# Kernel tuning notes

Hardware: AMD Instinct MI355X
Metric: run time of the kernel (lower is better)

Reference implementation:

```python
import jax, jax.numpy as jnp
import numpy as np

# NSAFlowLayer config (from init_kwargs)
W_ORTHO = 0.5      # w: blend weight of soft-polar retraction
MAX_ITER = 50      # max_iter (run fixed-length under jit; tol check omitted)
LR = 0.1           # 'default' initial learning rate for the fidelity gradient step
NS_ITERS = 8       # Newton-Schulz iterations for the (k,k) inverse matrix sqrt
EPS = 1e-8

B, P, K = 32, 16384, 64


def _invsqrt_ns(M):
    """Differentiable inverse sqrt of SPD (k,k) matrix via coupled Newton-Schulz."""
    k = M.shape[0]
    I = jnp.eye(k, dtype=M.dtype)
    nrm = jnp.trace(M) + EPS
    Y = M / nrm
    Z = I
    for _ in range(NS_ITERS):  # small fixed loop over k x k mats
        T = 0.5 * (3.0 * I - Z @ Y)
        Y = Y @ T
        Z = T @ Z
    return Z / jnp.sqrt(nrm)  # approx M^{-1/2}


def _nsa_flow_single(x0):
    """One independent NSA flow: gradient step on 0.5||Y-X0||^2, soft-polar
    retraction toward the Stiefel manifold, nonnegativity projection."""
    def step(Y, _):
        G = Y - x0                      # fidelity gradient (p,k)
        Y = Y - LR * G                  # gradient step
        S = _invsqrt_ns(Y.T @ Y)        # (k,k) inverse sqrt of Gram matrix
        Y = (1.0 - W_ORTHO) * Y + W_ORTHO * (Y @ S)  # soft polar retraction
        Y = jnp.maximum(Y, 0.0)         # nonneg projection
        return Y, None
    Yf, _ = jax.lax.scan(step, x0, None, length=MAX_ITER)  # Y0 = X0
    return Yf


def setup_inputs() -> dict:
    key = jax.random.key(0)
    X0 = jax.random.uniform(key, (B, P, K), dtype=jnp.float32)
    return {"X0": X0}


def reference(X0) -> jnp.ndarray:
    return jax.vmap(_nsa_flow_single)(X0)  # (B, p, k)
```

## Files before the change

kernel.cpp:

```cpp
#include <hip/hip_runtime.h>


#define BATCH 32
#define NP    16384
#define NK    64
#define NITER 50
#define NSIT  8
#define EPSC  1e-8f
#define CH    64
#define NT    256
#define NTNS  512
#define SP    68

#define FMA16(D, A0, A1, A2, A3, BV) do {                                  \
  D[0][0] = fmaf(A0, BV.x, D[0][0]); D[0][1] = fmaf(A0, BV.y, D[0][1]);    \
  D[0][2] = fmaf(A0, BV.z, D[0][2]); D[0][3] = fmaf(A0, BV.w, D[0][3]);    \
  D[1][0] = fmaf(A1, BV.x, D[1][0]); D[1][1] = fmaf(A1, BV.y, D[1][1]);    \
  D[1][2] = fmaf(A1, BV.z, D[1][2]); D[1][3] = fmaf(A1, BV.w, D[1][3]);    \
  D[2][0] = fmaf(A2, BV.x, D[2][0]); D[2][1] = fmaf(A2, BV.y, D[2][1]);    \
  D[2][2] = fmaf(A2, BV.z, D[2][2]); D[2][3] = fmaf(A2, BV.w, D[2][3]);    \
  D[3][0] = fmaf(A3, BV.x, D[3][0]); D[3][1] = fmaf(A3, BV.y, D[3][1]);    \
  D[3][2] = fmaf(A3, BV.z, D[3][2]); D[3][3] = fmaf(A3, BV.w, D[3][3]);    \
} while (0)

#define FMA8(D, A0, A1, BV) do {                                           \
  D[0][0] = fmaf(A0, BV.x, D[0][0]); D[0][1] = fmaf(A0, BV.y, D[0][1]);    \
  D[0][2] = fmaf(A0, BV.z, D[0][2]); D[0][3] = fmaf(A0, BV.w, D[0][3]);    \
  D[1][0] = fmaf(A1, BV.x, D[1][0]); D[1][1] = fmaf(A1, BV.y, D[1][1]);    \
  D[1][2] = fmaf(A1, BV.z, D[1][2]); D[1][3] = fmaf(A1, BV.w, D[1][3]);    \
} while (0)

__device__ __forceinline__ void gram_acc(const float (*sZ)[SP], int i0, int j0,
                                         float (&acc)[4][4]) {
#pragma unroll 4
  for (int r = 0; r < CH; ++r) {
    float4 zi = *(const float4*)&sZ[r][i0];
    float4 zj = *(const float4*)&sZ[r][j0];
    FMA16(acc, zi.x, zi.y, zi.z, zi.w, zj);
  }
}

__global__ __launch_bounds__(NT, 4) void k_init(const float* __restrict__ X0,
                                                float* __restrict__ Y,
                                                float* __restrict__ partials,
                                                int shift) {
  __shared__ float sZ[CH][SP];
  const int tid = threadIdx.x, blk = blockIdx.x;
  const int bpb = 1 << shift;
  const int b = blk >> shift, rb = blk & (bpb - 1);
  const int rpb = NP >> shift, nch = rpb / CH;
  const size_t base = ((size_t)b * NP + (size_t)rb * rpb) * NK;
  const float* __restrict__ x0 = X0 + base;
  float* __restrict__ y = Y + base;
  const int it = tid >> 4, jt = tid & 15;
  const int i0 = it * 4, j0 = jt * 4;
  float acc[4][4] = {{0.f}};

  for (int ch = 0; ch < nch; ++ch) {
    const float* xo = x0 + ch * CH * NK;
    float* yo = y + ch * CH * NK;
#pragma unroll
    for (int q = 0; q < 4; ++q) {
      int fi = (q * NT + tid) * 4;
      float4 xv = *(const float4*)(xo + fi);
      *(float4*)(yo + fi) = xv;
      int r = fi >> 6, c = fi & 63;
      *(float4*)&sZ[r][c] = xv;
    }
    __syncthreads();
    gram_acc(sZ, i0, j0, acc);
    __syncthreads();
  }
  float* p = partials + (size_t)blk * NK * NK;
#pragma unroll
  for (int a = 0; a < 4; ++a)
    *(float4*)(p + (i0 + a) * NK + j0) =
        make_float4(acc[a][0], acc[a][1], acc[a][2], acc[a][3]);
}

__global__ __launch_bounds__(NTNS, 2) void k_ns(const float* __restrict__ partials,
                                                float* __restrict__ S,
                                                int npart) {
  __shared__ float sA[NK][SP];
  __shared__ float sB[NK][SP];
  __shared__ float sT[NK][SP];
  __shared__ float sRed[8];

  const int tid = threadIdx.x, b = blockIdx.x;
  const int it = tid >> 4, jt = tid & 15;
  const int i0 = it * 2, j0 = jt * 4;

  float m[2][4] = {{0.f}};
  const float* pb = partials + (size_t)b * npart * NK * NK;
#pragma unroll 4
  for (int p = 0; p < npart; ++p) {
    const float* pp = pb + p * NK * NK;
#pragma unroll
    for (int a = 0; a < 2; ++a) {
      float4 v = *(const float4*)(pp + (i0 + a) * NK + j0);
      m[a][0] += v.x; m[a][1] += v.y; m[a][2] += v.z; m[a][3] += v.w;
    }
  }
  float local = 0.f;
#pragma unroll
  for (int a = 0; a < 2; ++a)
#pragma unroll
    for (int c = 0; c < 4; ++c)
      if ((i0 + a) == (j0 + c)) local += m[a][c];
#pragma unroll
  for (int off = 32; off; off >>= 1) local += __shfl_down(local, off);
  if ((tid & 63) == 0) sRed[tid >> 6] = local;
  __syncthreads();
  float nrm = EPSC;
#pragma unroll
  for (int w = 0; w < 8; ++w) nrm += sRed[w];
  const float inv = 1.0f / nrm;

#pragma unroll
  for (int a = 0; a < 2; ++a)
#pragma unroll
    for (int c = 0; c < 4; ++c) {
      sA[i0 + a][j0 + c] = m[a][c] * inv;
      sB[i0 + a][j0 + c] = (i0 + a) == (j0 + c) ? 1.0f : 0.0f;
    }
  __syncthreads();

  {
#pragma unroll
    for (int a = 0; a < 2; ++a)
#pragma unroll
      for (int c = 0; c < 4; ++c)
        sT[i0 + a][j0 + c] =
            (((i0 + a) == (j0 + c)) ? 1.5f : 0.0f) - 0.5f * sA[i0 + a][j0 + c];
    __syncthreads();
    float r1[2][4] = {{0.f}};
#pragma unroll 4
    for (int k = 0; k < NK; ++k) {
      float y0 = sA[i0 + 0][k], y1 = sA[i0 + 1][k];
      float4 tv = *(const float4*)&sT[k][j0];
      FMA8(r1, y0, y1, tv);
    }
    __syncthreads();
#pragma unroll
    for (int a = 0; a < 2; ++a)
#pragma unroll
      for (int c = 0; c < 4; ++c) {
        sA[i0 + a][j0 + c] = r1[a][c];
        sB[i0 + a][j0 + c] = sT[i0 + a][j0 + c];
      }
    __syncthreads();
  }

  for (int ns = 1; ns < NSIT; ++ns) {
    float d[2][4] = {{0.f}};
#pragma unroll 4
    for (int k = 0; k < NK; ++k) {
      float b0 = sB[i0 + 0][k], b1 = sB[i0 + 1][k];
      float4 av = *(const float4*)&sA[k][j0];
      FMA8(d, b0, b1, av);
    }
#pragma unroll
    for (int a = 0; a < 2; ++a)
#pragma unroll
      for (int c = 0; c < 4; ++c)
        sT[i0 + a][j0 + c] =
            (((i0 + a) == (j0 + c)) ? 1.5f : 0.0f) - 0.5f * d[a][c];
    __syncthreads();

    float r1[2][4] = {{0.f}}, r2[2][4] = {{0.f}};
#pragma unroll 4
    for (int k = 0; k < NK; ++k) {
      float y0 = sA[i0 + 0][k], y1 = sA[i0 + 1][k];
      float4 tv = *(const float4*)&sT[k][j0];
      FMA8(r1, y0, y1, tv);
      float t0 = sT[i0 + 0][k], t1 = sT[i0 + 1][k];
      float4 zv = *(const float4*)&sB[k][j0];
      FMA8(r2, t0, t1, zv);
    }
    __syncthreads();
#pragma unroll
    for (int a = 0; a < 2; ++a)
#pragma unroll
      for (int c = 0; c < 4; ++c) {
        sA[i0 + a][j0 + c] = r1[a][c];
        sB[i0 + a][j0 + c] = r2[a][c];
      }
    __syncthreads();
  }

  const float sc = 1.0f / sqrtf(nrm);
  float* Sb = S + (size_t)b * NK * NK;
#pragma unroll
  for (int a = 0; a < 2; ++a) {
    float4 v = make_float4(sB[i0 + a][j0 + 0] * sc, sB[i0 + a][j0 + 1] * sc,
                           sB[i0 + a][j0 + 2] * sc, sB[i0 + a][j0 + 3] * sc);
    *(float4*)(Sb + (i0 + a) * NK + j0) = v;
  }
}

__global__ __launch_bounds__(NT, 4) void k_fused(const float* __restrict__ X0,
                                                 float* __restrict__ Y,
                                                 const float* __restrict__ S,
                                                 float* __restrict__ partials,
                                                 int last, int shift) {
  __shared__ float sS[NK][NK];
  __shared__ float sYp[CH][SP];

  const int tid = threadIdx.x, blk = blockIdx.x;
  const int bpb = 1 << shift;
  const int b = blk >> shift, rb = blk & (bpb - 1);
  const int rpb = NP >> shift, nch = rpb / CH;
  const size_t base = ((size_t)b * NP + (size_t)rb * rpb) * NK;
  const float* __restrict__ x0 = X0 + base;
  float* __restrict__ y = Y + base;

  {
    const float4* Sb = (const float4*)(S + (size_t)b * NK * NK);
    float4* d = (float4*)sS;
    for (int i = tid; i < NK * NK / 4; i += NT) d[i] = Sb[i];
  }

  const int it = tid >> 4, jt = tid & 15;
  const int i0 = it * 4, j0 = jt * 4;
  float acc[4][4] = {{0.f}};
  __syncthreads();

  for (int ch = 0; ch < nch; ++ch) {
    const float* xo = x0 + ch * CH * NK;
    float* yo = y + ch * CH * NK;

#pragma unroll
    for (int q = 0; q < 4; ++q) {
      int fi = (q * NT + tid) * 4;
      int r = fi >> 6, c = fi & 63;
      float4 yv = *(const float4*)(yo + fi);
      float4 xv = *(const float4*)(xo + fi);
      float4 yp;
      yp.x = fmaf(0.9f, yv.x, 0.1f * xv.x);
      yp.y = fmaf(0.9f, yv.y, 0.1f * xv.y);
      yp.z = fmaf(0.9f, yv.z, 0.1f * xv.z);
      yp.w = fmaf(0.9f, yv.w, 0.1f * xv.w);
      *(float4*)&sYp[r][c] = yp;
    }
    __syncthreads();

    float dot[4][4] = {{0.f}};
#pragma unroll 4
    for (int k = 0; k < NK; ++k) {
      float a0 = sYp[i0 + 0][k], a1 = sYp[i0 + 1][k];
      float a2 = sYp[i0 + 2][k], a3 = sYp[i0 + 3][k];
      float4 bv = *(const float4*)&sS[k][j0];
      FMA16(dot, a0, a1, a2, a3, bv);
    }
    __syncthreads();

#pragma unroll
    for (int a = 0; a < 4; ++a) {
      int r = i0 + a;
      float4 ypv = *(const float4*)&sYp[r][j0];
      float4 yn;
      yn.x = fmaxf(fmaf(0.5f, ypv.x, 0.5f * dot[a][0]), 0.f);
      yn.y = fmaxf(fmaf(0.5f, ypv.y, 0.5f * dot[a][1]), 0.f);
      yn.z = fmaxf(fmaf(0.5f, ypv.z, 0.5f * dot[a][2]), 0.f);
      yn.w = fmaxf(fmaf(0.5f, ypv.w, 0.5f * dot[a][3]), 0.f);
      *(float4*)(yo + r * NK + j0) = yn;
      if (!last) {
        float4 xv = *(const float4*)(xo + r * NK + j0);
        float4 z;
        z.x = fmaf(0.9f, yn.x, 0.1f * xv.x);
        z.y = fmaf(0.9f, yn.y, 0.1f * xv.y);
        z.z = fmaf(0.9f, yn.z, 0.1f * xv.z);
        z.w = fmaf(0.9f, yn.w, 0.1f * xv.w);
        *(float4*)&sYp[r][j0] = z;
      }
    }
    __syncthreads();
    if (!last) gram_acc(sYp, i0, j0, acc);
    __syncthreads();
  }

  if (!last) {
    float* p = partials + (size_t)blk * NK * NK;
#pragma unroll
    for (int a = 0; a < 4; ++a)
      *(float4*)(p + (i0 + a) * NK + j0) =
          make_float4(acc[a][0], acc[a][1], acc[a][2], acc[a][3]);
  }
}

extern "C" void kernel_launch(void* const* d_in, const int* in_sizes, int n_in,
                              void* d_out, int out_size, void* d_ws,
                              size_t ws_size, hipStream_t stream) {
  (void)in_sizes; (void)n_in; (void)out_size;
  const float* X0 = (const float*)d_in[0];
  float* Y = (float*)d_out;

  const size_t needed5 =
      ((size_t)(BATCH << 5) + BATCH) * NK * NK * sizeof(float);
  const int shift = (ws_size >= needed5) ? 5 : 4;
  const int nblk = BATCH << shift;

  float* partials = (float*)d_ws;
  float* S = partials + (size_t)nblk * NK * NK;

  k_init<<<nblk, NT, 0, stream>>>(X0, Y, partials, shift);
  for (int t = 0; t < NITER; ++t) {
    k_ns<<<BATCH, NTNS, 0, stream>>>(partials, S, 1 << shift);
    k_fused<<<nblk, NT, 0, stream>>>(X0, Y, S, partials,
                                     t == NITER - 1 ? 1 : 0, shift);
  }
}
```

Before: 9.877 ms.

## Add parallel partial-Gram reduction kernel and exploit Gram symmetry in fused kernel

Adds a k_red kernel that pre-reduces the per-block Gram partials into four groups per batch using 128 blocks, so k_ns, which runs only 32 blocks, sums four slots instead of all of them. In k_fused, the Gram accumulation now computes only upper-triangular 4x4 tiles, splitting each off-diagonal tile across two threads, and mirrors the results when writing to halve the FMA work. Also raises unroll factors in several inner loops. Costs an extra kernel launch per iteration and uses scattered transposed stores for the partials.

```diff
diff --git a/kernel.cpp b/kernel.cpp
--- a/kernel.cpp
+++ b/kernel.cpp
@@ -11,6 +11,7 @@
 #define NT    256
 #define NTNS  512
 #define SP    68
+#define NRED  4
 
 #define FMA16(D, A0, A1, A2, A3, BV) do {                                  \
   D[0][0] = fmaf(A0, BV.x, D[0][0]); D[0][1] = fmaf(A0, BV.y, D[0][1]);    \
@@ -32,7 +33,7 @@
 
 __device__ __forceinline__ void gram_acc(const float (*sZ)[SP], int i0, int j0,
                                          float (&acc)[4][4]) {
-#pragma unroll 4
+#pragma unroll 8
   for (int r = 0; r < CH; ++r) {
     float4 zi = *(const float4*)&sZ[r][i0];
     float4 zj = *(const float4*)&sZ[r][j0];
@@ -78,9 +79,27 @@
         make_float4(acc[a][0], acc[a][1], acc[a][2], acc[a][3]);
 }
 
+__global__ __launch_bounds__(NT, 8) void k_red(float* __restrict__ partials,
+                                               int per_group, int bpb) {
+  const int blk = blockIdx.x, tid = threadIdx.x;
+  const int b = blk >> 2, g = blk & 3;
+  float4* base = (float4*)partials +
+                 ((size_t)b * bpb + (size_t)g * per_group) * (NK * NK / 4);
+#pragma unroll
+  for (int q = 0; q < 4; ++q) {
+    int e = q * NT + tid;
+    float4 s = base[e];
+    for (int p = 1; p < per_group; ++p) {
+      float4 v = base[(size_t)p * (NK * NK / 4) + e];
+      s.x += v.x; s.y += v.y; s.z += v.z; s.w += v.w;
+    }
+    base[e] = s;
+  }
+}
+
 __global__ __launch_bounds__(NTNS, 2) void k_ns(const float* __restrict__ partials,
                                                 float* __restrict__ S,
-                                                int npart) {
+                                                int per_group, int bpb) {
   __shared__ float sA[NK][SP];
   __shared__ float sB[NK][SP];
   __shared__ float sT[NK][SP];
@@ -91,10 +110,10 @@
   const int i0 = it * 2, j0 = jt * 4;
 
   float m[2][4] = {{0.f}};
-  const float* pb = partials + (size_t)b * npart * NK * NK;
-#pragma unroll 4
-  for (int p = 0; p < npart; ++p) {
-    const float* pp = pb + p * NK * NK;
+  const float* pb = partials + (size_t)b * bpb * NK * NK;
+#pragma unroll
+  for (int g = 0; g < NRED; ++g) {
+    const float* pp = pb + (size_t)g * per_group * NK * NK;
 #pragma unroll
     for (int a = 0; a < 2; ++a) {
       float4 v = *(const float4*)(pp + (i0 + a) * NK + j0);
@@ -134,7 +153,7 @@
             (((i0 + a) == (j0 + c)) ? 1.5f : 0.0f) - 0.5f * sA[i0 + a][j0 + c];
     __syncthreads();
     float r1[2][4] = {{0.f}};
-#pragma unroll 4
+#pragma unroll 8
     for (int k = 0; k < NK; ++k) {
       float y0 = sA[i0 + 0][k], y1 = sA[i0 + 1][k];
       float4 tv = *(const float4*)&sT[k][j0];
@@ -153,7 +172,7 @@
 
   for (int ns = 1; ns < NSIT; ++ns) {
     float d[2][4] = {{0.f}};
-#pragma unroll 4
+#pragma unroll 8
     for (int k = 0; k < NK; ++k) {
       float b0 = sB[i0 + 0][k], b1 = sB[i0 + 1][k];
       float4 av = *(const float4*)&sA[k][j0];
@@ -168,7 +187,7 @@
     __syncthreads();
 
     float r1[2][4] = {{0.f}}, r2[2][4] = {{0.f}};
-#pragma unroll 4
+#pragma unroll 8
     for (int k = 0; k < NK; ++k) {
       float y0 = sA[i0 + 0][k], y1 = sA[i0 + 1][k];
       float4 tv = *(const float4*)&sT[k][j0];
@@ -222,6 +241,22 @@
 
   const int it = tid >> 4, jt = tid & 15;
   const int i0 = it * 4, j0 = jt * 4;
+
+  int g_ti, g_tj;
+  bool g_diag;
+  {
+    if (tid >= 240) { g_diag = true; g_ti = g_tj = tid - 240; }
+    else {
+      g_diag = false;
+      int p = tid >> 1;
+      int t = 0, cum = 0;
+      while (cum + (15 - t) <= p) { cum += 15 - t; ++t; }
+      g_ti = t; g_tj = t + 1 + (p - cum);
+    }
+  }
+  const int gr0 = g_ti * 4 + (g_diag ? 0 : (tid & 1) * 2);
+  const int gc0 = g_tj * 4;
+
   float acc[4][4] = {{0.f}};
   __syncthreads();
 
@@ -245,7 +280,7 @@
     __syncthreads();
 
     float dot[4][4] = {{0.f}};
-#pragma unroll 4
+#pragma unroll 8
     for (int k = 0; k < NK; ++k) {
       float a0 = sYp[i0 + 0][k], a1 = sYp[i0 + 1][k];
       float a2 = sYp[i0 + 2][k], a3 = sYp[i0 + 3][k];
@@ -275,16 +310,44 @@
       }
     }
     __syncthreads();
-    if (!last) gram_acc(sYp, i0, j0, acc);
+
+    if (!last) {
+      if (g_diag) {
+#pragma unroll 8
+        for (int r = 0; r < CH; ++r) {
+          float4 z = *(const float4*)&sYp[r][gc0];
+          FMA16(acc, z.x, z.y, z.z, z.w, z);
+        }
+      } else {
+#pragma unroll 8
+        for (int r = 0; r < CH; ++r) {
+          float a0 = sYp[r][gr0], a1 = sYp[r][gr0 + 1];
+          float4 zb = *(const float4*)&sYp[r][gc0];
+          FMA8(acc, a0, a1, zb);
+        }
+      }
+    }
     __syncthreads();
   }
 
   if (!last) {
     float* p = partials + (size_t)blk * NK * NK;
-#pragma unroll
-    for (int a = 0; a < 4; ++a)
-      *(float4*)(p + (i0 + a) * NK + j0) =
-          make_float4(acc[a][0], acc[a][1], acc[a][2], acc[a][3]);
+    if (g_diag) {
+#pragma unroll
+      for (int a = 0; a < 4; ++a)
+        *(float4*)(p + (gr0 + a) * NK + gc0) =
+            make_float4(acc[a][0], acc[a][1], acc[a][2], acc[a][3]);
+    } else {
+#pragma unroll
+      for (int a = 0; a < 2; ++a)
+        *(float4*)(p + (gr0 + a) * NK + gc0) =
+            make_float4(acc[a][0], acc[a][1], acc[a][2], acc[a][3]);
+#pragma unroll
+      for (int c = 0; c < 4; ++c) {
+        p[(gc0 + c) * NK + gr0 + 0] = acc[0][c];
+        p[(gc0 + c) * NK + gr0 + 1] = acc[1][c];
+      }
+    }
   }
 }
 
@@ -295,17 +358,20 @@
   const float* X0 = (const float*)d_in[0];
   float* Y = (float*)d_out;
 
-  const size_t needed5 =
-      ((size_t)(BATCH << 5) + BATCH) * NK * NK * sizeof(float);
+  const size_t slotf = (size_t)NK * NK;
+  const size_t needed5 = (((size_t)BATCH << 5) + BATCH) * slotf * sizeof(float);
   const int shift = (ws_size >= needed5) ? 5 : 4;
   const int nblk = BATCH << shift;
+  const int bpb = 1 << shift;
+  const int per_group = bpb / NRED;
 
   float* partials = (float*)d_ws;
-  float* S = partials + (size_t)nblk * NK * NK;
+  float* S = partials + (size_t)nblk * slotf;
 
   k_init<<<nblk, NT, 0, stream>>>(X0, Y, partials, shift);
   for (int t = 0; t < NITER; ++t) {
-    k_ns<<<BATCH, NTNS, 0, stream>>>(partials, S, 1 << shift);
+    k_red<<<BATCH * NRED, NT, 0, stream>>>(partials, per_group, bpb);
+    k_ns<<<BATCH, NTNS, 0, stream>>>(partials, S, per_group, bpb);
     k_fused<<<nblk, NT, 0, stream>>>(X0, Y, S, partials,
                                      t == NITER - 1 ? 1 : 0, shift);
   }
```

Result: slower. 10.48 ms (+6.1%).

## Use split-fp16 MFMA for Y·S and Gram accumulation in fused kernel

Applied to the files above, without the earlier changes.

Replaces the scalar FP32 FMA matmuls in the fused per-iteration kernel (Y·S projection and the Y^T Y Gram partials) with MFMA 16x16x32 fp16 instructions. Each operand is split into a hi/lo fp16 pair (lo scaled by 2048) and three MFMAs emulate near-fp32 accuracy. S is emitted by the NS kernel as transposed hi/lo fp16 arrays. It also bumps a few unroll factors. The extra conversion work, the transposed LDS stores (likely bank conflicts), and the reduced precision are traded for matrix-core throughput.

```diff
diff --git a/kernel.cpp b/kernel.cpp
--- a/kernel.cpp
+++ b/kernel.cpp
@@ -11,6 +11,13 @@
 #define NT    256
 #define NTNS  512
 #define SP    68
+#define SPH   72
+
+using h4   = __attribute__((ext_vector_type(4))) _Float16;
+using h8   = __attribute__((ext_vector_type(8))) _Float16;
+using f32x4 = __attribute__((ext_vector_type(4))) float;
+
+#define MFMA16x32(A, B, C) __builtin_amdgcn_mfma_f32_16x16x32_f16(A, B, C, 0, 0, 0)
 
 #define FMA16(D, A0, A1, A2, A3, BV) do {                                  \
   D[0][0] = fmaf(A0, BV.x, D[0][0]); D[0][1] = fmaf(A0, BV.y, D[0][1]);    \
@@ -32,7 +39,7 @@
 
 __device__ __forceinline__ void gram_acc(const float (*sZ)[SP], int i0, int j0,
                                          float (&acc)[4][4]) {
-#pragma unroll 4
+#pragma unroll 8
   for (int r = 0; r < CH; ++r) {
     float4 zi = *(const float4*)&sZ[r][i0];
     float4 zj = *(const float4*)&sZ[r][j0];
@@ -79,7 +86,8 @@
 }
 
 __global__ __launch_bounds__(NTNS, 2) void k_ns(const float* __restrict__ partials,
-                                                float* __restrict__ S,
+                                                _Float16* __restrict__ Sthi,
+                                                _Float16* __restrict__ Stlo,
                                                 int npart) {
   __shared__ float sA[NK][SP];
   __shared__ float sB[NK][SP];
@@ -94,7 +102,7 @@
   const float* pb = partials + (size_t)b * npart * NK * NK;
 #pragma unroll 4
   for (int p = 0; p < npart; ++p) {
-    const float* pp = pb + p * NK * NK;
+    const float* pp = pb + (size_t)p * NK * NK;
 #pragma unroll
     for (int a = 0; a < 2; ++a) {
       float4 v = *(const float4*)(pp + (i0 + a) * NK + j0);
@@ -134,7 +142,7 @@
             (((i0 + a) == (j0 + c)) ? 1.5f : 0.0f) - 0.5f * sA[i0 + a][j0 + c];
     __syncthreads();
     float r1[2][4] = {{0.f}};
-#pragma unroll 4
+#pragma unroll 8
     for (int k = 0; k < NK; ++k) {
       float y0 = sA[i0 + 0][k], y1 = sA[i0 + 1][k];
       float4 tv = *(const float4*)&sT[k][j0];
@@ -153,7 +161,7 @@
 
   for (int ns = 1; ns < NSIT; ++ns) {
     float d[2][4] = {{0.f}};
-#pragma unroll 4
+#pragma unroll 8
     for (int k = 0; k < NK; ++k) {
       float b0 = sB[i0 + 0][k], b1 = sB[i0 + 1][k];
       float4 av = *(const float4*)&sA[k][j0];
@@ -168,7 +176,7 @@
     __syncthreads();
 
     float r1[2][4] = {{0.f}}, r2[2][4] = {{0.f}};
-#pragma unroll 4
+#pragma unroll 8
     for (int k = 0; k < NK; ++k) {
       float y0 = sA[i0 + 0][k], y1 = sA[i0 + 1][k];
       float4 tv = *(const float4*)&sT[k][j0];
@@ -189,22 +197,27 @@
   }
 
   const float sc = 1.0f / sqrtf(nrm);
-  float* Sb = S + (size_t)b * NK * NK;
-#pragma unroll
-  for (int a = 0; a < 2; ++a) {
-    float4 v = make_float4(sB[i0 + a][j0 + 0] * sc, sB[i0 + a][j0 + 1] * sc,
-                           sB[i0 + a][j0 + 2] * sc, sB[i0 + a][j0 + 3] * sc);
-    *(float4*)(Sb + (i0 + a) * NK + j0) = v;
-  }
-}
-
-__global__ __launch_bounds__(NT, 4) void k_fused(const float* __restrict__ X0,
-                                                 float* __restrict__ Y,
-                                                 const float* __restrict__ S,
-                                                 float* __restrict__ partials,
-                                                 int last, int shift) {
-  __shared__ float sS[NK][NK];
-  __shared__ float sYp[CH][SP];
+  _Float16* Sh = Sthi + (size_t)b * NK * NK;
+  _Float16* Sl = Stlo + (size_t)b * NK * NK;
+#pragma unroll
+  for (int a = 0; a < 2; ++a)
+#pragma unroll
+    for (int c = 0; c < 4; ++c) {
+      float s = sB[i0 + a][j0 + c] * sc;
+      _Float16 hh = (_Float16)s;
+      Sh[(j0 + c) * NK + (i0 + a)] = hh;
+      Sl[(j0 + c) * NK + (i0 + a)] = (_Float16)((s - (float)hh) * 2048.f);
+    }
+}
+
+__global__ __launch_bounds__(NT, 4) void k_fused(
+    const float* __restrict__ X0, float* __restrict__ Y,
+    const _Float16* __restrict__ Sthi, const _Float16* __restrict__ Stlo,
+    float* __restrict__ partials, int last, int shift) {
+  __shared__ _Float16 sYa[CH][SPH];
+  __shared__ _Float16 sYb[CH][SPH];
+  __shared__ _Float16 sSa[NK][SPH];
+  __shared__ _Float16 sSb[NK][SPH];
 
   const int tid = threadIdx.x, blk = blockIdx.x;
   const int bpb = 1 << shift;
@@ -215,14 +228,26 @@
   float* __restrict__ y = Y + base;
 
   {
-    const float4* Sb = (const float4*)(S + (size_t)b * NK * NK);
-    float4* d = (float4*)sS;
-    for (int i = tid; i < NK * NK / 4; i += NT) d[i] = Sb[i];
-  }
-
-  const int it = tid >> 4, jt = tid & 15;
-  const int i0 = it * 4, j0 = jt * 4;
-  float acc[4][4] = {{0.f}};
+    const _Float16* sh = Sthi + (size_t)b * NK * NK;
+    const _Float16* sl = Stlo + (size_t)b * NK * NK;
+    int r = tid >> 2, c = (tid & 3) * 16;
+    const uint4* gh = (const uint4*)(sh + r * NK + c);
+    const uint4* gl = (const uint4*)(sl + r * NK + c);
+    uint4* dh = (uint4*)&sSa[r][c];
+    uint4* dl = (uint4*)&sSb[r][c];
+    dh[0] = gh[0]; dh[1] = gh[1];
+    dl[0] = gl[0]; dl[1] = gl[1];
+  }
+
+  const int wv = tid >> 6, ln = tid & 63;
+  const int lr = ln & 15, lq = ln >> 4;
+
+  f32x4 gacc[4], glo[4];
+#pragma unroll
+  for (int t = 0; t < 4; ++t) {
+    gacc[t] = (f32x4){0.f, 0.f, 0.f, 0.f};
+    glo[t]  = (f32x4){0.f, 0.f, 0.f, 0.f};
+  }
   __syncthreads();
 
   for (int ch = 0; ch < nch; ++ch) {
@@ -235,56 +260,99 @@
       int r = fi >> 6, c = fi & 63;
       float4 yv = *(const float4*)(yo + fi);
       float4 xv = *(const float4*)(xo + fi);
-      float4 yp;
-      yp.x = fmaf(0.9f, yv.x, 0.1f * xv.x);
-      yp.y = fmaf(0.9f, yv.y, 0.1f * xv.y);
-      yp.z = fmaf(0.9f, yv.z, 0.1f * xv.z);
-      yp.w = fmaf(0.9f, yv.w, 0.1f * xv.w);
-      *(float4*)&sYp[r][c] = yp;
-    }
-    __syncthreads();
-
-    float dot[4][4] = {{0.f}};
-#pragma unroll 4
-    for (int k = 0; k < NK; ++k) {
-      float a0 = sYp[i0 + 0][k], a1 = sYp[i0 + 1][k];
-      float a2 = sYp[i0 + 2][k], a3 = sYp[i0 + 3][k];
-      float4 bv = *(const float4*)&sS[k][j0];
-      FMA16(dot, a0, a1, a2, a3, bv);
-    }
-    __syncthreads();
-
-#pragma unroll
-    for (int a = 0; a < 4; ++a) {
-      int r = i0 + a;
-      float4 ypv = *(const float4*)&sYp[r][j0];
-      float4 yn;
-      yn.x = fmaxf(fmaf(0.5f, ypv.x, 0.5f * dot[a][0]), 0.f);
-      yn.y = fmaxf(fmaf(0.5f, ypv.y, 0.5f * dot[a][1]), 0.f);
-      yn.z = fmaxf(fmaf(0.5f, ypv.z, 0.5f * dot[a][2]), 0.f);
-      yn.w = fmaxf(fmaf(0.5f, ypv.w, 0.5f * dot[a][3]), 0.f);
-      *(float4*)(yo + r * NK + j0) = yn;
-      if (!last) {
-        float4 xv = *(const float4*)(xo + r * NK + j0);
-        float4 z;
-        z.x = fmaf(0.9f, yn.x, 0.1f * xv.x);
-        z.y = fmaf(0.9f, yn.y, 0.1f * xv.y);
-        z.z = fmaf(0.9f, yn.z, 0.1f * xv.z);
-        z.w = fmaf(0.9f, yn.w, 0.1f * xv.w);
-        *(float4*)&sYp[r][j0] = z;
-      }
-    }
-    __syncthreads();
-    if (!last) gram_acc(sYp, i0, j0, acc);
+      float p0 = fmaf(0.9f, yv.x, 0.1f * xv.x);
+      float p1 = fmaf(0.9f, yv.y, 0.1f * xv.y);
+      float p2 = fmaf(0.9f, yv.z, 0.1f * xv.z);
+      float p3 = fmaf(0.9f, yv.w, 0.1f * xv.w);
+      _Float16 h0 = (_Float16)p0, h1 = (_Float16)p1;
+      _Float16 h2 = (_Float16)p2, h3 = (_Float16)p3;
+      *(h4*)&sYa[r][c] = (h4){h0, h1, h2, h3};
+      *(h4*)&sYb[r][c] = (h4){(_Float16)((p0 - (float)h0) * 2048.f),
+                              (_Float16)((p1 - (float)h1) * 2048.f),
+                              (_Float16)((p2 - (float)h2) * 2048.f),
+                              (_Float16)((p3 - (float)h3) * 2048.f)};
+    }
+    __syncthreads();
+
+    h8 a_hi[2], a_lo[2];
+#pragma unroll
+    for (int kh = 0; kh < 2; ++kh) {
+      a_hi[kh] = *(const h8*)&sYa[16 * wv + lr][lq * 8 + 32 * kh];
+      a_lo[kh] = *(const h8*)&sYb[16 * wv + lr][lq * 8 + 32 * kh];
+    }
+    f32x4 dot[4];
+    float ypv[4][4];
+#pragma unroll
+    for (int tc = 0; tc < 4; ++tc) {
+      f32x4 ah = (f32x4){0.f, 0.f, 0.f, 0.f};
+      f32x4 al = (f32x4){0.f, 0.f, 0.f, 0.f};
+#pragma unroll
+      for (int kh = 0; kh < 2; ++kh) {
+        h8 b_hi = *(const h8*)&sSa[16 * tc + lr][lq * 8 + 32 * kh];
+        h8 b_lo = *(const h8*)&sSb[16 * tc + lr][lq * 8 + 32 * kh];
+        ah = MFMA16x32(a_hi[kh], b_hi, ah);
+        al = MFMA16x32(a_hi[kh], b_lo, al);
+        al = MFMA16x32(a_lo[kh], b_hi, al);
+      }
+      dot[tc] = ah + al * (1.f / 2048.f);
+#pragma unroll
+      for (int r_ = 0; r_ < 4; ++r_) {
+        int R = 16 * wv + 4 * lq + r_, C = 16 * tc + lr;
+        ypv[tc][r_] = (float)sYa[R][C] + (float)sYb[R][C] * (1.f / 2048.f);
+      }
+    }
+    __syncthreads();
+
+#pragma unroll
+    for (int tc = 0; tc < 4; ++tc) {
+#pragma unroll
+      for (int r_ = 0; r_ < 4; ++r_) {
+        int R = 16 * wv + 4 * lq + r_, C = 16 * tc + lr;
+        float yn = fmaxf(0.5f * ypv[tc][r_] + 0.5f * dot[tc][r_], 0.f);
+        yo[R * NK + C] = yn;
+        if (!last) {
+          float z = fmaf(0.9f, yn, 0.1f * xo[R * NK + C]);
+          _Float16 zh = (_Float16)z;
+          sYa[C][R] = zh;
+          sYb[C][R] = (_Float16)((z - (float)zh) * 2048.f);
+        }
+      }
+    }
+    __syncthreads();
+
+    if (!last) {
+      h8 ga_hi[2], ga_lo[2];
+#pragma unroll
+      for (int kh = 0; kh < 2; ++kh) {
+        ga_hi[kh] = *(const h8*)&sYa[16 * wv + lr][lq * 8 + 32 * kh];
+        ga_lo[kh] = *(const h8*)&sYb[16 * wv + lr][lq * 8 + 32 * kh];
+      }
+#pragma unroll
+      for (int tc = 0; tc < 4; ++tc) {
+        f32x4 lt = (f32x4){0.f, 0.f, 0.f, 0.f};
+#pragma unroll
+        for (int kh = 0; kh < 2; ++kh) {
+          h8 gb_hi = *(const h8*)&sYa[16 * tc + lr][lq * 8 + 32 * kh];
+          h8 gb_lo = *(const h8*)&sYb[16 * tc + lr][lq * 8 + 32 * kh];
+          gacc[tc] = MFMA16x32(ga_hi[kh], gb_hi, gacc[tc]);
+          lt = MFMA16x32(ga_hi[kh], gb_lo, lt);
+          lt = MFMA16x32(ga_lo[kh], gb_hi, lt);
+        }
+        glo[tc] += lt;
+      }
+    }
     __syncthreads();
   }
 
   if (!last) {
     float* p = partials + (size_t)blk * NK * NK;
 #pragma unroll
-    for (int a = 0; a < 4; ++a)
-      *(float4*)(p + (i0 + a) * NK + j0) =
-          make_float4(acc[a][0], acc[a][1], acc[a][2], acc[a][3]);
+    for (int tc = 0; tc < 4; ++tc)
+#pragma unroll
+      for (int r_ = 0; r_ < 4; ++r_) {
+        int R = 16 * wv + 4 * lq + r_, C = 16 * tc + lr;
+        p[R * NK + C] = gacc[tc][r_] + glo[tc][r_] * (1.f / 2048.f);
+      }
   }
 }
 
@@ -295,18 +363,20 @@
   const float* X0 = (const float*)d_in[0];
   float* Y = (float*)d_out;
 
-  const size_t needed5 =
-      ((size_t)(BATCH << 5) + BATCH) * NK * NK * sizeof(float);
-  const int shift = (ws_size >= needed5) ? 5 : 4;
+  const size_t slotf = (size_t)NK * NK;
+  const size_t need5 = ((size_t)(BATCH << 5)) * slotf * 4
+                       + 2 * (size_t)BATCH * slotf * 2;
+  const int shift = (ws_size >= need5) ? 5 : 4;
   const int nblk = BATCH << shift;
 
   float* partials = (float*)d_ws;
-  float* S = partials + (size_t)nblk * NK * NK;
+  _Float16* Sthi = (_Float16*)((char*)d_ws + (size_t)nblk * slotf * 4);
+  _Float16* Stlo = Sthi + (size_t)BATCH * slotf;
 
   k_init<<<nblk, NT, 0, stream>>>(X0, Y, partials, shift);
   for (int t = 0; t < NITER; ++t) {
-    k_ns<<<BATCH, NTNS, 0, stream>>>(partials, S, 1 << shift);
-    k_fused<<<nblk, NT, 0, stream>>>(X0, Y, S, partials,
+    k_ns<<<BATCH, NTNS, 0, stream>>>(partials, Sthi, Stlo, 1 << shift);
+    k_fused<<<nblk, NT, 0, stream>>>(X0, Y, Sthi, Stlo, partials,
                                      t == NITER - 1 ? 1 : 0, shift);
   }
 }
```

Result: faster. 8.595 ms (-13.0%).
